# Kernel tuning notes

Hardware: AMD Instinct MI355X
Metric: run time of the kernel (lower is better)

The kernel has to match this reference:

```python
import jax, jax.numpy as jnp
import numpy as np

VOC, TOPIC, EMB, BATCH = 128000, 512, 1024, 1024

def setup_inputs() -> dict:
    key = jax.random.key(0)
    k1, k2, k3 = jax.random.split(key, 3)
    x = jax.random.normal(k1, (TOPIC, BATCH), dtype=jnp.float32)
    beta0 = jax.random.normal(k2, (VOC, EMB), dtype=jnp.float32)
    beta_t = jax.random.normal(k3, (TOPIC, EMB), dtype=jnp.float32) * 0.02  # nn.init.normal_(std=0.02)
    return {"x": x, "beta0": beta0, "beta_t": beta_t, "t": 0}

def reference(x, beta0, beta_t, t):
    # w: [voc, topic] = beta0 [voc, emb] @ beta_t.T [emb, topic]
    # (the t==0 branch and else branch are identical in the source)
    w = jnp.einsum('ve,te->vt', beta0, beta_t)
    w = jax.nn.softmax(w, axis=0)  # softmax over vocab dim (dim=0)
    # out: [voc, batch]
    return jnp.einsum('vt,tb->vb', w, x)
```

## Files before the change

### kernel.cpp

```cpp
#include <hip/hip_runtime.h>

typedef _Float16 f16x8 __attribute__((ext_vector_type(8)));
typedef float    f32x4 __attribute__((ext_vector_type(4)));
typedef unsigned short u16;

#define VOC   128000
#define TOPIC 512
#define EMB   1024
#define BATCH 1024

#define BM 128
#define BN 128
#define BK 64
#define ROWB (BK * 2)

__device__ __forceinline__ int swz(int row, int kbyte) {
    return row * ROWB + (kbyte ^ ((row & 7) << 4));
}

union H2U { _Float16 h; u16 u; };

__device__ __forceinline__ int xcd_swz(int bid, int nwg) {
    return (bid & 7) * (nwg >> 3) + (bid >> 3);
}

__global__ __launch_bounds__(256) void gemm1_kernel(
    const float* __restrict__ beta0, const float* __restrict__ betat,
    u16* __restrict__ EgBase, size_t tile_stride, float* __restrict__ sg)
{
    __shared__ char lds[(BM + BN) * BK * 2];
    char* ldsA = lds;
    char* ldsB = lds + BM * BK * 2;

    const int tid  = threadIdx.x;
    const int slot = tid & 7;
    const int srow = tid >> 3;
    const int lane = tid & 63;
    const int wid  = tid >> 6;
    const int wr = wid >> 1, wc = wid & 1;
    const int lr = lane & 15, lk = lane >> 4;

    const int bid = xcd_swz(blockIdx.x, gridDim.x);
    const int t0 = (bid & 3) * BN;
    const int v0 = (bid >> 2) * BM;

    f32x4 acc[4][4] = {};
    float4 rA0[4], rA1[4], rB0[4], rB1[4];

    auto load_tiles = [&](int kt) {
        const int k0 = kt * BK;
        #pragma unroll
        for (int p = 0; p < 4; ++p) {
            const float4* gA = reinterpret_cast<const float4*>(
                beta0 + (size_t)(v0 + p * 32 + srow) * EMB + k0 + slot * 8);
            rA0[p] = gA[0]; rA1[p] = gA[1];
            const float4* gB = reinterpret_cast<const float4*>(
                betat + (size_t)(t0 + p * 32 + srow) * EMB + k0 + slot * 8);
            rB0[p] = gB[0]; rB1[p] = gB[1];
        }
    };

    load_tiles(0);

    for (int kt = 0; kt < EMB / BK; ++kt) {
        __syncthreads();
        #pragma unroll
        for (int p = 0; p < 4; ++p) {
            const int row = p * 32 + srow;
            f16x8 h;
            h[0] = (_Float16)rA0[p].x; h[1] = (_Float16)rA0[p].y;
            h[2] = (_Float16)rA0[p].z; h[3] = (_Float16)rA0[p].w;
            h[4] = (_Float16)rA1[p].x; h[5] = (_Float16)rA1[p].y;
            h[6] = (_Float16)rA1[p].z; h[7] = (_Float16)rA1[p].w;
            *reinterpret_cast<f16x8*>(ldsA + swz(row, slot * 16)) = h;
            f16x8 g;
            g[0] = (_Float16)rB0[p].x; g[1] = (_Float16)rB0[p].y;
            g[2] = (_Float16)rB0[p].z; g[3] = (_Float16)rB0[p].w;
            g[4] = (_Float16)rB1[p].x; g[5] = (_Float16)rB1[p].y;
            g[6] = (_Float16)rB1[p].z; g[7] = (_Float16)rB1[p].w;
            *reinterpret_cast<f16x8*>(ldsB + swz(row, slot * 16)) = g;
        }
        if (kt + 1 < EMB / BK) load_tiles(kt + 1);
        __syncthreads();
        #pragma unroll
        for (int ks = 0; ks < 2; ++ks) {
            f16x8 af[4], bf[4];
            #pragma unroll
            for (int m = 0; m < 4; ++m) {
                const int row = wr * 64 + m * 16 + lr;
                af[m] = *reinterpret_cast<const f16x8*>(ldsA + swz(row, ks * 64 + lk * 16));
            }
            #pragma unroll
            for (int n = 0; n < 4; ++n) {
                const int row = wc * 64 + n * 16 + lr;
                bf[n] = *reinterpret_cast<const f16x8*>(ldsB + swz(row, ks * 64 + lk * 16));
            }
            #pragma unroll
            for (int m = 0; m < 4; ++m)
                #pragma unroll
                for (int n = 0; n < 4; ++n)
                    acc[m][n] = __builtin_amdgcn_mfma_f32_16x16x32_f16(
                        af[m], bf[n], acc[m][n], 0, 0, 0);
        }
    }

    __syncthreads();
    u16* ldsE = reinterpret_cast<u16*>(lds);
    #pragma unroll
    for (int m = 0; m < 4; ++m)
      #pragma unroll
      for (int n = 0; n < 4; ++n)
        #pragma unroll
        for (int r = 0; r < 4; ++r) {
            const int row = wr * 64 + m * 16 + lk * 4 + r;
            const int col = wc * 64 + n * 16 + lr;
            H2U cv; cv.h = (_Float16)__expf(acc[m][n][r]);
            ldsE[row * BN + col] = cv.u;
        }
    __syncthreads();

    {
        const int row = tid >> 1, half = tid & 1;
        u16* dst = EgBase + (size_t)(v0 / BM) * tile_stride
                 + (size_t)row * TOPIC + t0 + half * 64;
        #pragma unroll
        for (int i = 0; i < 8; ++i) {
            int4 vv = *reinterpret_cast<const int4*>(&ldsE[row * BN + half * 64 + i * 8]);
            *reinterpret_cast<int4*>(dst + i * 8) = vv;
        }
    }
    if (tid < BN) {
        float sum = 0.f;
        for (int r = 0; r < BM; ++r) {
            H2U cv; cv.u = ldsE[r * BN + tid];
            sum += (float)cv.h;
        }
        atomicAdd(sg + t0 + tid, sum);
    }
}

__global__ void xst_kernel(const float* __restrict__ x, const float* __restrict__ s,
                           u16* __restrict__ xsT)
{
    __shared__ float tile[32][33];
    const int b0 = blockIdx.x * 32, t0 = blockIdx.y * 32;
    const int tx = threadIdx.x, ty = threadIdx.y;
    tile[ty][tx] = x[(size_t)(t0 + ty) * BATCH + b0 + tx];
    __syncthreads();
    const float sc = 65536.0f / s[t0 + tx];
    H2U cv; cv.h = (_Float16)(tile[tx][ty] * sc);
    xsT[(size_t)(b0 + ty) * TOPIC + t0 + tx] = cv.u;
}

__global__ __launch_bounds__(256) void gemm2_kernel(
    const u16* __restrict__ EgBase, size_t tile_stride,
    const u16* __restrict__ xsT, float* __restrict__ out)
{
    __shared__ char lds[(BM + BN) * BK * 2];
    char* ldsA = lds;
    char* ldsB = lds + BM * BK * 2;

    const int tid  = threadIdx.x;
    const int lane = tid & 63;
    const int w    = tid >> 6;
    const int wr = w >> 1, wc = w & 1;
    const int lr = lane & 15, lk = lane >> 4;

    const int bid = xcd_swz(blockIdx.x, gridDim.x);
    const int b0 = (bid & 7) * BN;
    const int v0 = (bid >> 3) * BM;

    const u16* Et = EgBase + (size_t)(v0 / BM) * tile_stride;

    const int srow8  = lane >> 3;
    const int schunk = ((lane & 7) ^ srow8) * 8;

    f32x4 acc[4][4] = {};

    for (int kt = 0; kt < TOPIC / BK; ++kt) {
        const int k0 = kt * BK;
        __syncthreads();
        #pragma unroll
        for (int p = 0; p < 4; ++p) {
            const int rbase = p * 32 + w * 8;
            const u16* gA = Et + (size_t)(rbase + srow8) * TOPIC + k0 + schunk;
            __builtin_amdgcn_global_load_lds(
                (const __attribute__((address_space(1))) unsigned int*)gA,
                (__attribute__((address_space(3))) unsigned int*)(ldsA + rbase * ROWB),
                16, 0, 0);
            const u16* gB = xsT + (size_t)(b0 + rbase + srow8) * TOPIC + k0 + schunk;
            __builtin_amdgcn_global_load_lds(
                (const __attribute__((address_space(1))) unsigned int*)gB,
                (__attribute__((address_space(3))) unsigned int*)(ldsB + rbase * ROWB),
                16, 0, 0);
        }
        __syncthreads();
        #pragma unroll
        for (int ks = 0; ks < 2; ++ks) {
            f16x8 af[4], bf[4];
            #pragma unroll
            for (int m = 0; m < 4; ++m) {
                const int row = wr * 64 + m * 16 + lr;
                af[m] = *reinterpret_cast<const f16x8*>(ldsA + swz(row, ks * 64 + lk * 16));
            }
            #pragma unroll
            for (int n = 0; n < 4; ++n) {
                const int row = wc * 64 + n * 16 + lr;
                bf[n] = *reinterpret_cast<const f16x8*>(ldsB + swz(row, ks * 64 + lk * 16));
            }
            #pragma unroll
            for (int m = 0; m < 4; ++m)
                #pragma unroll
                for (int n = 0; n < 4; ++n)
                    acc[m][n] = __builtin_amdgcn_mfma_f32_16x16x32_f16(
                        af[m], bf[n], acc[m][n], 0, 0, 0);
        }
    }

    #pragma unroll
    for (int m = 0; m < 4; ++m)
      #pragma unroll
      for (int n = 0; n < 4; ++n)
        #pragma unroll
        for (int r = 0; r < 4; ++r) {
            const int row = wr * 64 + m * 16 + lk * 4 + r;
            const int col = wc * 64 + n * 16 + lr;
            out[(size_t)(v0 + row) * BATCH + b0 + col] = acc[m][n][r] * 0x1p-16f;
        }
}

__global__ __launch_bounds__(512) void gemm2_fused_kernel(
    const u16* __restrict__ EgBase,
    const u16* __restrict__ xsT, float* __restrict__ out)
{
    __shared__ char ldsB[BN * BK * 2];

    const int tid  = threadIdx.x;
    const int lane = tid & 63;
    const int wid  = tid >> 6;
    const int wr = wid >> 2, wc = wid & 3;
    const int lr = lane & 15, lk = lane >> 4;

    const size_t tile = blockIdx.x;
    const u16* Et = EgBase + tile * (size_t)(BM * BATCH * 2);

    f16x8 af[4][16];
    #pragma unroll
    for (int m = 0; m < 4; ++m) {
        const int row = wr * 64 + m * 16 + lr;
        #pragma unroll
        for (int kb = 0; kb < 16; ++kb)
            af[m][kb] = *reinterpret_cast<const f16x8*>(
                Et + (size_t)row * TOPIC + kb * 32 + lk * 8);
    }
    asm volatile("s_waitcnt vmcnt(0)" ::: "memory");
    __syncthreads();

    for (int bc = 0; bc < 8; ++bc) {
        f32x4 acc[4][2] = {};
        #pragma unroll
        for (int ks = 0; ks < 8; ++ks) {
            __syncthreads();
            {
                const int srow = tid >> 2;
                const int slot = (tid & 3) * 2;
                const u16* g = xsT + (size_t)(bc * 128 + srow) * TOPIC + ks * 64 + slot * 8;
                int4 v0 = *reinterpret_cast<const int4*>(g);
                int4 v1 = *reinterpret_cast<const int4*>(g + 8);
                *reinterpret_cast<int4*>(ldsB + swz(srow, slot * 16)) = v0;
                *reinterpret_cast<int4*>(ldsB + swz(srow, (slot + 1) * 16)) = v1;
            }
            __syncthreads();
            #pragma unroll
            for (int kk = 0; kk < 2; ++kk) {
                f16x8 bf[2];
                #pragma unroll
                for (int n = 0; n < 2; ++n) {
                    const int row = wc * 32 + n * 16 + lr;
                    bf[n] = *reinterpret_cast<const f16x8*>(ldsB + swz(row, kk * 64 + lk * 16));
                }
                #pragma unroll
                for (int m = 0; m < 4; ++m)
                    #pragma unroll
                    for (int n = 0; n < 2; ++n)
                        acc[m][n] = __builtin_amdgcn_mfma_f32_16x16x32_f16(
                            af[m][ks * 2 + kk], bf[n], acc[m][n], 0, 0, 0);
            }
        }
        #pragma unroll
        for (int m = 0; m < 4; ++m)
          #pragma unroll
          for (int n = 0; n < 2; ++n)
            #pragma unroll
            for (int r = 0; r < 4; ++r) {
                const int row = wr * 64 + m * 16 + lk * 4 + r;
                const int col = wc * 32 + n * 16 + lr;
                out[(tile * BM + row) * BATCH + bc * 128 + col] = acc[m][n][r] * 0x1p-16f;
            }
    }
}

extern "C" void kernel_launch(void* const* d_in, const int* in_sizes, int n_in,
                              void* d_out, int out_size, void* d_ws, size_t ws_size,
                              hipStream_t stream)
{
    const float* x     = (const float*)d_in[0];
    const float* beta0 = (const float*)d_in[1];
    const float* betat = (const float*)d_in[2];
    float* out = (float*)d_out;

    const size_t E_OFF    = 2u * 1024u * 1024u;
    const size_t need_big = E_OFF + (size_t)VOC * TOPIC * 2;
    const size_t need_min = 4096 + (size_t)BATCH * TOPIC * 2;
    if (ws_size < need_min) return;

    float* s_g = (float*)d_ws;
    u16*   xsT = (u16*)((char*)d_ws + 4096);

    hipMemsetAsync(d_ws, 0, 2048, stream);

    if (ws_size >= need_big) {
        u16* Eg = (u16*)((char*)d_ws + E_OFF);
        const size_t tstride = (size_t)BM * TOPIC;

        gemm1_kernel<<<dim3((TOPIC / BN) * (VOC / BM)), 256, 0, stream>>>(
            beta0, betat, Eg, tstride, s_g);

        dim3 gp(BATCH / 32, TOPIC / 32);
        xst_kernel<<<gp, dim3(32, 32), 0, stream>>>(x, s_g, xsT);

        gemm2_kernel<<<dim3((BATCH / BN) * (VOC / BM)), 256, 0, stream>>>(
            Eg, tstride, xsT, out);
    } else {
        u16* Eg = (u16*)d_out;
        const size_t tstride = (size_t)BM * BATCH * 2;

        gemm1_kernel<<<dim3((TOPIC / BN) * (VOC / BM)), 256, 0, stream>>>(
            beta0, betat, Eg, tstride, s_g);

        dim3 gp(BATCH / 32, TOPIC / 32);
        xst_kernel<<<gp, dim3(32, 32), 0, stream>>>(x, s_g, xsT);

        gemm2_fused_kernel<<<dim3(VOC / BM), 512, 0, stream>>>(Eg, xsT, out);
    }
}
```

Measured before the change: 630.9 us.

## Pre-convert beta_t to fp16, enlarge GEMM tiles to 128x256 with 512 threads

Adds a small kernel that converts beta_t to fp16 once, so gemm1 loads its B operand straight into LDS with global_load_lds instead of converting fp32 in registers in every block. Both GEMMs move to 512-thread blocks with 128x256 output tiles, which halves the number of blocks and raises reuse of each A tile. The gemm1 epilogue is split into two halves to fit LDS. The in-place fallback path is restructured into a chunked gemm2a plus a gemm2b for the last column chunk. The larger tiles raise register and LDS pressure and may lower occupancy, and the extra conversion launch adds a little overhead.

```diff
diff --git a/kernel.cpp b/kernel.cpp
--- a/kernel.cpp
+++ b/kernel.cpp
@@ -8,93 +8,92 @@
 #define TOPIC 512
 #define EMB   1024
 #define BATCH 1024
-
-#define BM 128
-#define BN 128
-#define BK 64
-#define ROWB (BK * 2)
+#define ROWB  128
 
 __device__ __forceinline__ int swz(int row, int kbyte) {
     return row * ROWB + (kbyte ^ ((row & 7) << 4));
 }
-
-union H2U { _Float16 h; u16 u; };
-
 __device__ __forceinline__ int xcd_swz(int bid, int nwg) {
     return (bid & 7) * (nwg >> 3) + (bid >> 3);
 }
-
-__global__ __launch_bounds__(256) void gemm1_kernel(
-    const float* __restrict__ beta0, const float* __restrict__ betat,
-    u16* __restrict__ EgBase, size_t tile_stride, float* __restrict__ sg)
-{
-    __shared__ char lds[(BM + BN) * BK * 2];
+union H2U { _Float16 h; u16 u; };
+
+__global__ void cvt_betat_kernel(const float* __restrict__ betat, u16* __restrict__ bt16) {
+    const size_t g = (size_t)blockIdx.x * 256 + threadIdx.x;
+    const float4* src = reinterpret_cast<const float4*>(betat) + g * 2;
+    float4 a = src[0], b = src[1];
+    f16x8 h;
+    h[0]=(_Float16)a.x; h[1]=(_Float16)a.y; h[2]=(_Float16)a.z; h[3]=(_Float16)a.w;
+    h[4]=(_Float16)b.x; h[5]=(_Float16)b.y; h[6]=(_Float16)b.z; h[7]=(_Float16)b.w;
+    *(reinterpret_cast<f16x8*>(bt16) + g) = h;
+}
+
+__global__ __launch_bounds__(512, 2) void gemm1_kernel(
+    const float* __restrict__ beta0, const u16* __restrict__ bt16,
+    u16* __restrict__ Eg, size_t TSTR, int RSTR, float* __restrict__ sg)
+{
+    __shared__ char lds[49152];
     char* ldsA = lds;
-    char* ldsB = lds + BM * BK * 2;
+    char* ldsB = lds + 16384;
 
     const int tid  = threadIdx.x;
-    const int slot = tid & 7;
-    const int srow = tid >> 3;
     const int lane = tid & 63;
     const int wid  = tid >> 6;
-    const int wr = wid >> 1, wc = wid & 1;
+    const int wr = wid >> 2, wc = wid & 3;
     const int lr = lane & 15, lk = lane >> 4;
-
-    const int bid = xcd_swz(blockIdx.x, gridDim.x);
-    const int t0 = (bid & 3) * BN;
-    const int v0 = (bid >> 2) * BM;
+    const int srow8  = lane >> 3;
+    const int schunk = ((lane & 7) ^ srow8) * 8;
+
+    const int bid  = xcd_swz(blockIdx.x, gridDim.x);
+    const int t0   = (bid & 1) * 256;
+    const int tile = bid >> 1;
+    const int v0   = tile * 128;
+
+    const int arow = tid >> 2;
+    const int asp  = (tid & 3) * 2;
 
     f32x4 acc[4][4] = {};
-    float4 rA0[4], rA1[4], rB0[4], rB1[4];
-
-    auto load_tiles = [&](int kt) {
-        const int k0 = kt * BK;
+    float4 rA[4];
+
+    auto loadA = [&](int kt) {
+        const float4* g = reinterpret_cast<const float4*>(
+            beta0 + (size_t)(v0 + arow) * EMB + kt * 64 + asp * 8);
+        rA[0] = g[0]; rA[1] = g[1]; rA[2] = g[2]; rA[3] = g[3];
+    };
+
+    loadA(0);
+
+    for (int kt = 0; kt < EMB / 64; ++kt) {
+        __syncthreads();
+        const u16* bsrc = bt16 + (size_t)(t0 + wid * 8 + srow8) * EMB + kt * 64 + schunk;
         #pragma unroll
         for (int p = 0; p < 4; ++p) {
-            const float4* gA = reinterpret_cast<const float4*>(
-                beta0 + (size_t)(v0 + p * 32 + srow) * EMB + k0 + slot * 8);
-            rA0[p] = gA[0]; rA1[p] = gA[1];
-            const float4* gB = reinterpret_cast<const float4*>(
-                betat + (size_t)(t0 + p * 32 + srow) * EMB + k0 + slot * 8);
-            rB0[p] = gB[0]; rB1[p] = gB[1];
-        }
-    };
-
-    load_tiles(0);
-
-    for (int kt = 0; kt < EMB / BK; ++kt) {
-        __syncthreads();
-        #pragma unroll
-        for (int p = 0; p < 4; ++p) {
-            const int row = p * 32 + srow;
+            __builtin_amdgcn_global_load_lds(
+                (const __attribute__((address_space(1))) unsigned int*)(bsrc + (size_t)p * 64 * EMB),
+                (__attribute__((address_space(3))) unsigned int*)(ldsB + (p * 64 + wid * 8) * ROWB),
+                16, 0, 0);
+        }
+        {
             f16x8 h;
-            h[0] = (_Float16)rA0[p].x; h[1] = (_Float16)rA0[p].y;
-            h[2] = (_Float16)rA0[p].z; h[3] = (_Float16)rA0[p].w;
-            h[4] = (_Float16)rA1[p].x; h[5] = (_Float16)rA1[p].y;
-            h[6] = (_Float16)rA1[p].z; h[7] = (_Float16)rA1[p].w;
-            *reinterpret_cast<f16x8*>(ldsA + swz(row, slot * 16)) = h;
-            f16x8 g;
-            g[0] = (_Float16)rB0[p].x; g[1] = (_Float16)rB0[p].y;
-            g[2] = (_Float16)rB0[p].z; g[3] = (_Float16)rB0[p].w;
-            g[4] = (_Float16)rB1[p].x; g[5] = (_Float16)rB1[p].y;
-            g[6] = (_Float16)rB1[p].z; g[7] = (_Float16)rB1[p].w;
-            *reinterpret_cast<f16x8*>(ldsB + swz(row, slot * 16)) = g;
-        }
-        if (kt + 1 < EMB / BK) load_tiles(kt + 1);
+            h[0]=(_Float16)rA[0].x; h[1]=(_Float16)rA[0].y; h[2]=(_Float16)rA[0].z; h[3]=(_Float16)rA[0].w;
+            h[4]=(_Float16)rA[1].x; h[5]=(_Float16)rA[1].y; h[6]=(_Float16)rA[1].z; h[7]=(_Float16)rA[1].w;
+            *reinterpret_cast<f16x8*>(ldsA + swz(arow, asp * 16)) = h;
+            f16x8 h2;
+            h2[0]=(_Float16)rA[2].x; h2[1]=(_Float16)rA[2].y; h2[2]=(_Float16)rA[2].z; h2[3]=(_Float16)rA[2].w;
+            h2[4]=(_Float16)rA[3].x; h2[5]=(_Float16)rA[3].y; h2[6]=(_Float16)rA[3].z; h2[7]=(_Float16)rA[3].w;
+            *reinterpret_cast<f16x8*>(ldsA + swz(arow, (asp + 1) * 16)) = h2;
+        }
+        if (kt + 1 < EMB / 64) loadA(kt + 1);
         __syncthreads();
         #pragma unroll
         for (int ks = 0; ks < 2; ++ks) {
             f16x8 af[4], bf[4];
             #pragma unroll
-            for (int m = 0; m < 4; ++m) {
-                const int row = wr * 64 + m * 16 + lr;
-                af[m] = *reinterpret_cast<const f16x8*>(ldsA + swz(row, ks * 64 + lk * 16));
-            }
-            #pragma unroll
-            for (int n = 0; n < 4; ++n) {
-                const int row = wc * 64 + n * 16 + lr;
-                bf[n] = *reinterpret_cast<const f16x8*>(ldsB + swz(row, ks * 64 + lk * 16));
-            }
+            for (int m = 0; m < 4; ++m)
+                af[m] = *reinterpret_cast<const f16x8*>(ldsA + swz(wr * 64 + m * 16 + lr, ks * 64 + lk * 16));
+            #pragma unroll
+            for (int n = 0; n < 4; ++n)
+                bf[n] = *reinterpret_cast<const f16x8*>(ldsB + swz(wc * 64 + n * 16 + lr, ks * 64 + lk * 16));
             #pragma unroll
             for (int m = 0; m < 4; ++m)
                 #pragma unroll
@@ -106,37 +105,39 @@
 
     __syncthreads();
     u16* ldsE = reinterpret_cast<u16*>(lds);
+    float csum = 0.f;
     #pragma unroll
-    for (int m = 0; m < 4; ++m)
-      #pragma unroll
-      for (int n = 0; n < 4; ++n)
-        #pragma unroll
-        for (int r = 0; r < 4; ++r) {
-            const int row = wr * 64 + m * 16 + lk * 4 + r;
-            const int col = wc * 64 + n * 16 + lr;
-            H2U cv; cv.h = (_Float16)__expf(acc[m][n][r]);
-            ldsE[row * BN + col] = cv.u;
-        }
-    __syncthreads();
-
-    {
-        const int row = tid >> 1, half = tid & 1;
-        u16* dst = EgBase + (size_t)(v0 / BM) * tile_stride
-                 + (size_t)row * TOPIC + t0 + half * 64;
-        #pragma unroll
-        for (int i = 0; i < 8; ++i) {
-            int4 vv = *reinterpret_cast<const int4*>(&ldsE[row * BN + half * 64 + i * 8]);
-            *reinterpret_cast<int4*>(dst + i * 8) = vv;
-        }
-    }
-    if (tid < BN) {
-        float sum = 0.f;
-        for (int r = 0; r < BM; ++r) {
-            H2U cv; cv.u = ldsE[r * BN + tid];
-            sum += (float)cv.h;
-        }
-        atomicAdd(sg + t0 + tid, sum);
-    }
+    for (int c = 0; c < 2; ++c) {
+        if (wr == c) {
+            #pragma unroll
+            for (int m = 0; m < 4; ++m)
+              #pragma unroll
+              for (int n = 0; n < 4; ++n)
+                #pragma unroll
+                for (int r = 0; r < 4; ++r) {
+                    const int row = m * 16 + lk * 4 + r;
+                    const int col = wc * 64 + n * 16 + lr;
+                    H2U cv; cv.h = (_Float16)__expf(acc[m][n][r]);
+                    ldsE[row * 264 + col] = cv.u;
+                }
+        }
+        __syncthreads();
+        {
+            const int row8 = tid >> 3, seg = tid & 7;
+            const int4* srcp = reinterpret_cast<const int4*>(&ldsE[row8 * 264 + seg * 32]);
+            u16* dst = Eg + tile * TSTR + (size_t)(c * 64 + row8) * RSTR + t0 + seg * 32;
+            int4 v0v = srcp[0], v1v = srcp[1], v2v = srcp[2], v3v = srcp[3];
+            int4* dp = reinterpret_cast<int4*>(dst);
+            dp[0] = v0v; dp[1] = v1v; dp[2] = v2v; dp[3] = v3v;
+        }
+        if (tid < 256) {
+            float s = 0.f;
+            for (int r = 0; r < 64; ++r) { H2U cv; cv.u = ldsE[r * 264 + tid]; s += (float)cv.h; }
+            csum += s;
+        }
+        __syncthreads();
+    }
+    if (tid < 256) atomicAdd(sg + t0 + tid, csum);
 }
 
 __global__ void xst_kernel(const float* __restrict__ x, const float* __restrict__ s,
@@ -152,152 +153,152 @@
     xsT[(size_t)(b0 + ty) * TOPIC + t0 + tx] = cv.u;
 }
 
-__global__ __launch_bounds__(256) void gemm2_kernel(
-    const u16* __restrict__ EgBase, size_t tile_stride,
-    const u16* __restrict__ xsT, float* __restrict__ out)
-{
-    __shared__ char lds[(BM + BN) * BK * 2];
+__global__ __launch_bounds__(512, 2) void gemm2a_kernel(
+    const u16* __restrict__ Eg, size_t TSTR, int RSTR,
+    const u16* __restrict__ xsT, float* __restrict__ out, int c0, int nch)
+{
+    __shared__ char lds[49152];
     char* ldsA = lds;
-    char* ldsB = lds + BM * BK * 2;
-
-    const int tid  = threadIdx.x;
-    const int lane = tid & 63;
-    const int w    = tid >> 6;
-    const int wr = w >> 1, wc = w & 1;
-    const int lr = lane & 15, lk = lane >> 4;
-
-    const int bid = xcd_swz(blockIdx.x, gridDim.x);
-    const int b0 = (bid & 7) * BN;
-    const int v0 = (bid >> 3) * BM;
-
-    const u16* Et = EgBase + (size_t)(v0 / BM) * tile_stride;
-
-    const int srow8  = lane >> 3;
-    const int schunk = ((lane & 7) ^ srow8) * 8;
-
-    f32x4 acc[4][4] = {};
-
-    for (int kt = 0; kt < TOPIC / BK; ++kt) {
-        const int k0 = kt * BK;
-        __syncthreads();
-        #pragma unroll
-        for (int p = 0; p < 4; ++p) {
-            const int rbase = p * 32 + w * 8;
-            const u16* gA = Et + (size_t)(rbase + srow8) * TOPIC + k0 + schunk;
-            __builtin_amdgcn_global_load_lds(
-                (const __attribute__((address_space(1))) unsigned int*)gA,
-                (__attribute__((address_space(3))) unsigned int*)(ldsA + rbase * ROWB),
-                16, 0, 0);
-            const u16* gB = xsT + (size_t)(b0 + rbase + srow8) * TOPIC + k0 + schunk;
-            __builtin_amdgcn_global_load_lds(
-                (const __attribute__((address_space(1))) unsigned int*)gB,
-                (__attribute__((address_space(3))) unsigned int*)(ldsB + rbase * ROWB),
-                16, 0, 0);
-        }
-        __syncthreads();
-        #pragma unroll
-        for (int ks = 0; ks < 2; ++ks) {
-            f16x8 af[4], bf[4];
-            #pragma unroll
-            for (int m = 0; m < 4; ++m) {
-                const int row = wr * 64 + m * 16 + lr;
-                af[m] = *reinterpret_cast<const f16x8*>(ldsA + swz(row, ks * 64 + lk * 16));
-            }
-            #pragma unroll
-            for (int n = 0; n < 4; ++n) {
-                const int row = wc * 64 + n * 16 + lr;
-                bf[n] = *reinterpret_cast<const f16x8*>(ldsB + swz(row, ks * 64 + lk * 16));
-            }
-            #pragma unroll
-            for (int m = 0; m < 4; ++m)
-                #pragma unroll
-                for (int n = 0; n < 4; ++n)
-                    acc[m][n] = __builtin_amdgcn_mfma_f32_16x16x32_f16(
-                        af[m], bf[n], acc[m][n], 0, 0, 0);
-        }
-    }
-
-    #pragma unroll
-    for (int m = 0; m < 4; ++m)
-      #pragma unroll
-      for (int n = 0; n < 4; ++n)
-        #pragma unroll
-        for (int r = 0; r < 4; ++r) {
-            const int row = wr * 64 + m * 16 + lk * 4 + r;
-            const int col = wc * 64 + n * 16 + lr;
-            out[(size_t)(v0 + row) * BATCH + b0 + col] = acc[m][n][r] * 0x1p-16f;
-        }
-}
-
-__global__ __launch_bounds__(512) void gemm2_fused_kernel(
-    const u16* __restrict__ EgBase,
-    const u16* __restrict__ xsT, float* __restrict__ out)
-{
-    __shared__ char ldsB[BN * BK * 2];
+    char* ldsB = lds + 16384;
 
     const int tid  = threadIdx.x;
     const int lane = tid & 63;
     const int wid  = tid >> 6;
     const int wr = wid >> 2, wc = wid & 3;
     const int lr = lane & 15, lk = lane >> 4;
-
-    const size_t tile = blockIdx.x;
-    const u16* Et = EgBase + tile * (size_t)(BM * BATCH * 2);
-
-    f16x8 af[4][16];
+    const int srow8  = lane >> 3;
+    const int schunk = ((lane & 7) ^ srow8) * 8;
+
+    const int bid   = xcd_swz(blockIdx.x, gridDim.x);
+    const int tile  = bid / nch;
+    const int chunk = bid % nch;
+    const int b0    = c0 + chunk * 256;
+    const int v0    = tile * 128;
+    const u16* Et   = Eg + tile * TSTR;
+
+    f32x4 acc[4][4] = {};
+
+    for (int kt = 0; kt < TOPIC / 64; ++kt) {
+        const int k0 = kt * 64;
+        __syncthreads();
+        #pragma unroll
+        for (int p = 0; p < 2; ++p) {
+            const int rbase = p * 64 + wid * 8;
+            __builtin_amdgcn_global_load_lds(
+                (const __attribute__((address_space(1))) unsigned int*)
+                    (Et + (size_t)(rbase + srow8) * RSTR + k0 + schunk),
+                (__attribute__((address_space(3))) unsigned int*)(ldsA + rbase * ROWB),
+                16, 0, 0);
+        }
+        #pragma unroll
+        for (int p = 0; p < 4; ++p) {
+            const int rbase = p * 64 + wid * 8;
+            __builtin_amdgcn_global_load_lds(
+                (const __attribute__((address_space(1))) unsigned int*)
+                    (xsT + (size_t)(b0 + rbase + srow8) * TOPIC + k0 + schunk),
+                (__attribute__((address_space(3))) unsigned int*)(ldsB + rbase * ROWB),
+                16, 0, 0);
+        }
+        __syncthreads();
+        #pragma unroll
+        for (int ks = 0; ks < 2; ++ks) {
+            f16x8 af[4], bf[4];
+            #pragma unroll
+            for (int m = 0; m < 4; ++m)
+                af[m] = *reinterpret_cast<const f16x8*>(ldsA + swz(wr * 64 + m * 16 + lr, ks * 64 + lk * 16));
+            #pragma unroll
+            for (int n = 0; n < 4; ++n)
+                bf[n] = *reinterpret_cast<const f16x8*>(ldsB + swz(wc * 64 + n * 16 + lr, ks * 64 + lk * 16));
+            #pragma unroll
+            for (int m = 0; m < 4; ++m)
+                #pragma unroll
+                for (int n = 0; n < 4; ++n)
+                    acc[m][n] = __builtin_amdgcn_mfma_f32_16x16x32_f16(
+                        af[m], bf[n], acc[m][n], 0, 0, 0);
+        }
+    }
+
     #pragma unroll
-    for (int m = 0; m < 4; ++m) {
-        const int row = wr * 64 + m * 16 + lr;
+    for (int m = 0; m < 4; ++m)
+      #pragma unroll
+      for (int n = 0; n < 4; ++n)
+        #pragma unroll
+        for (int r = 0; r < 4; ++r) {
+            const int row = wr * 64 + m * 16 + lk * 4 + r;
+            const int col = wc * 64 + n * 16 + lr;
+            out[(size_t)(v0 + row) * BATCH + b0 + col] = acc[m][n][r] * 0x1p-16f;
+        }
+}
+
+__global__ __launch_bounds__(512, 1) void gemm2b_kernel(
+    const u16* __restrict__ EgBase,
+    const u16* __restrict__ xsT, float* __restrict__ out)
+{
+    __shared__ char ldsB[32768];
+
+    const int tid  = threadIdx.x;
+    const int lane = tid & 63;
+    const int wid  = tid >> 6;
+    const int wr = wid >> 2, wc = wid & 3;
+    const int lr = lane & 15, lk = lane >> 4;
+
+    const int bid  = xcd_swz(blockIdx.x, gridDim.x);
+    const int tile = bid >> 1;
+    const int h    = bid & 1;
+    const u16* Et  = EgBase + (size_t)tile * 262144;
+
+    f16x8 af[2][16];
+    #pragma unroll
+    for (int m = 0; m < 2; ++m) {
+        const int row = h * 64 + wr * 32 + m * 16 + lr;
         #pragma unroll
         for (int kb = 0; kb < 16; ++kb)
             af[m][kb] = *reinterpret_cast<const f16x8*>(
-                Et + (size_t)row * TOPIC + kb * 32 + lk * 8);
+                Et + (size_t)row * 2048 + kb * 32 + lk * 8);
     }
     asm volatile("s_waitcnt vmcnt(0)" ::: "memory");
     __syncthreads();
 
-    for (int bc = 0; bc < 8; ++bc) {
-        f32x4 acc[4][2] = {};
-        #pragma unroll
-        for (int ks = 0; ks < 8; ++ks) {
-            __syncthreads();
-            {
-                const int srow = tid >> 2;
-                const int slot = (tid & 3) * 2;
-                const u16* g = xsT + (size_t)(bc * 128 + srow) * TOPIC + ks * 64 + slot * 8;
-                int4 v0 = *reinterpret_cast<const int4*>(g);
-                int4 v1 = *reinterpret_cast<const int4*>(g + 8);
-                *reinterpret_cast<int4*>(ldsB + swz(srow, slot * 16)) = v0;
-                *reinterpret_cast<int4*>(ldsB + swz(srow, (slot + 1) * 16)) = v1;
-            }
-            __syncthreads();
-            #pragma unroll
-            for (int kk = 0; kk < 2; ++kk) {
-                f16x8 bf[2];
+    f32x4 acc[2][4] = {};
+    for (int kt = 0; kt < 8; ++kt) {
+        __syncthreads();
+        {
+            const int srow = tid >> 1;
+            const int sp   = (tid & 1) * 4;
+            const u16* g = xsT + (size_t)srow * TOPIC + kt * 64 + sp * 8;
+            const int4* gv = reinterpret_cast<const int4*>(g);
+            int4 a = gv[0], b = gv[1], cc = gv[2], d = gv[3];
+            *reinterpret_cast<int4*>(ldsB + swz(srow, (sp + 0) * 16)) = a;
+            *reinterpret_cast<int4*>(ldsB + swz(srow, (sp + 1) * 16)) = b;
+            *reinterpret_cast<int4*>(ldsB + swz(srow, (sp + 2) * 16)) = cc;
+            *reinterpret_cast<int4*>(ldsB + swz(srow, (sp + 3) * 16)) = d;
+        }
+        __syncthreads();
+        #pragma unroll
+        for (int kk = 0; kk < 2; ++kk) {
+            f16x8 bf[4];
+            #pragma unroll
+            for (int n = 0; n < 4; ++n)
+                bf[n] = *reinterpret_cast<const f16x8*>(ldsB + swz(wc * 64 + n * 16 + lr, kk * 64 + lk * 16));
+            #pragma unroll
+            for (int m = 0; m < 2; ++m)
                 #pragma unroll
-                for (int n = 0; n < 2; ++n) {
-                    const int row = wc * 32 + n * 16 + lr;
-                    bf[n] = *reinterpret_cast<const f16x8*>(ldsB + swz(row, kk * 64 + lk * 16));
-                }
-                #pragma unroll
-                for (int m = 0; m < 4; ++m)
-                    #pragma unroll
-                    for (int n = 0; n < 2; ++n)
-                        acc[m][n] = __builtin_amdgcn_mfma_f32_16x16x32_f16(
-                            af[m][ks * 2 + kk], bf[n], acc[m][n], 0, 0, 0);
-            }
-        }
-        #pragma unroll
-        for (int m = 0; m < 4; ++m)
-          #pragma unroll
-          for (int n = 0; n < 2; ++n)
-            #pragma unroll
-            for (int r = 0; r < 4; ++r) {
-                const int row = wr * 64 + m * 16 + lk * 4 + r;
-                const int col = wc * 32 + n * 16 + lr;
-                out[(tile * BM + row) * BATCH + bc * 128 + col] = acc[m][n][r] * 0x1p-16f;
-            }
-    }
+                for (int n = 0; n < 4; ++n)
+                    acc[m][n] = __builtin_amdgcn_mfma_f32_16x16x32_f16(
+                        af[m][kt * 2 + kk], bf[n], acc[m][n], 0, 0, 0);
+        }
+    }
+
+    #pragma unroll
+    for (int m = 0; m < 2; ++m)
+      #pragma unroll
+      for (int n = 0; n < 4; ++n)
+        #pragma unroll
+        for (int r = 0; r < 4; ++r) {
+            const int row = h * 64 + wr * 32 + m * 16 + lk * 4 + r;
+            const int col = wc * 64 + n * 16 + lr;
+            out[((size_t)tile * 128 + row) * BATCH + col] = acc[m][n][r] * 0x1p-16f;
+        }
 }
 
 extern "C" void kernel_launch(void* const* d_in, const int* in_sizes, int n_in,
@@ -309,38 +310,27 @@
     const float* betat = (const float*)d_in[2];
     float* out = (float*)d_out;
 
-    const size_t E_OFF    = 2u * 1024u * 1024u;
-    const size_t need_big = E_OFF + (size_t)VOC * TOPIC * 2;
     const size_t need_min = 4096 + (size_t)BATCH * TOPIC * 2;
     if (ws_size < need_min) return;
-
-    float* s_g = (float*)d_ws;
-    u16*   xsT = (u16*)((char*)d_ws + 4096);
+    float* s_g  = (float*)d_ws;
+    u16*   buf1 = (u16*)((char*)d_ws + 4096);
+
+    const size_t E_OFF = 4u * 1024u * 1024u;
+    const bool big = ws_size >= E_OFF + (size_t)VOC * TOPIC * 2;
 
     hipMemsetAsync(d_ws, 0, 2048, stream);
-
-    if (ws_size >= need_big) {
-        u16* Eg = (u16*)((char*)d_ws + E_OFF);
-        const size_t tstride = (size_t)BM * TOPIC;
-
-        gemm1_kernel<<<dim3((TOPIC / BN) * (VOC / BM)), 256, 0, stream>>>(
-            beta0, betat, Eg, tstride, s_g);
-
-        dim3 gp(BATCH / 32, TOPIC / 32);
-        xst_kernel<<<gp, dim3(32, 32), 0, stream>>>(x, s_g, xsT);
-
-        gemm2_kernel<<<dim3((BATCH / BN) * (VOC / BM)), 256, 0, stream>>>(
-            Eg, tstride, xsT, out);
+    cvt_betat_kernel<<<256, 256, 0, stream>>>(betat, buf1);
+
+    if (big) {
+        u16* EgW = (u16*)((char*)d_ws + E_OFF);
+        gemm1_kernel<<<2000, 512, 0, stream>>>(beta0, buf1, EgW, (size_t)128 * 512, 512, s_g);
+        xst_kernel<<<dim3(BATCH / 32, TOPIC / 32), dim3(32, 32), 0, stream>>>(x, s_g, buf1);
+        gemm2a_kernel<<<4000, 512, 0, stream>>>(EgW, (size_t)128 * 512, 512, buf1, out, 0, 4);
     } else {
-        u16* Eg = (u16*)d_out;
-        const size_t tstride = (size_t)BM * BATCH * 2;
-
-        gemm1_kernel<<<dim3((TOPIC / BN) * (VOC / BM)), 256, 0, stream>>>(
-            beta0, betat, Eg, tstride, s_g);
-
-        dim3 gp(BATCH / 32, TOPIC / 32);
-        xst_kernel<<<gp, dim3(32, 32), 0, stream>>>(x, s_g, xsT);
-
-        gemm2_fused_kernel<<<dim3(VOC / BM), 512, 0, stream>>>(Eg, xsT, out);
-    }
-}
+        u16* EgO = (u16*)d_out;
+        gemm1_kernel<<<2000, 512, 0, stream>>>(beta0, buf1, EgO, (size_t)262144, 2048, s_g);
+        xst_kernel<<<dim3(BATCH / 32, TOPIC / 32), dim3(32, 32), 0, stream>>>(x, s_g, buf1);
+        gemm2a_kernel<<<3000, 512, 0, stream>>>(EgO, (size_t)262144, 2048, buf1, out, 256, 3);
+        gemm2b_kernel<<<2000, 512, 0, stream>>>(EgO, buf1, out);
+    }
+}
```

Measured after the change: 582.0 us. -7.8%, faster.
